# Kernel tuning notes

Hardware: AMD Instinct MI355X
Metric: run time of the kernel (lower is better)

## Reference

```python
import jax, jax.numpy as jnp
import numpy as np

B, S, E, H = 2, 2048, 1024, 16
D = E // H  # head_dim = 64


def _rope_angles(seq_len, d, dtype=jnp.float32):
    # standard RoPE frequencies: theta_i = 10000^{-2i/d}
    inv_freq = 1.0 / (10000.0 ** (jnp.arange(0, d, 2, dtype=dtype) / d))  # [d/2]
    pos = jnp.arange(seq_len, dtype=dtype)                                # [S]
    ang = pos[:, None] * inv_freq[None, :]                                # [S, d/2]
    ang = jnp.concatenate([ang, ang], axis=-1)                            # [S, d]
    return jnp.cos(ang), jnp.sin(ang)


def _rotate_half(t):
    t1, t2 = jnp.split(t, 2, axis=-1)
    return jnp.concatenate([-t2, t1], axis=-1)


def _apply_rope(t, cos, sin):
    # t: [B, H, S, D]; cos/sin: [S, D]
    return t * cos[None, None, :, :] + _rotate_half(t) * sin[None, None, :, :]


def setup_inputs() -> dict:
    key = jax.random.key(0)
    ks = jax.random.split(key, 6)
    x = jax.random.normal(ks[0], (B, S, E), dtype=jnp.float32)
    mask = jnp.tril(jnp.ones((S, S), dtype=bool))  # causal: True = attend
    scale = 1.0 / np.sqrt(E)
    Wq = jax.random.normal(ks[1], (E, E), dtype=jnp.float32) * scale
    Wk = jax.random.normal(ks[2], (E, E), dtype=jnp.float32) * scale
    Wv = jax.random.normal(ks[3], (E, E), dtype=jnp.float32) * scale
    Wo = jax.random.normal(ks[4], (E, E), dtype=jnp.float32) * scale
    z = jnp.zeros((E,), dtype=jnp.float32)
    return {"x": x, "mask": mask, "Wq": Wq, "bq": z, "Wk": Wk, "bk": z,
            "Wv": Wv, "bv": z, "Wo": Wo, "bo": z}


def reference(x, mask, Wq, bq, Wk, bk, Wv, bv, Wo, bo):
    b, s, e = x.shape
    # QKV projections (nn.Linear convention: y = x @ W.T + b)
    def proj(W, bias):
        y = jnp.einsum('bse,fe->bsf', x, W) + bias
        return y.reshape(b, s, H, D).transpose(0, 2, 1, 3)  # [B,H,S,D]
    q, k, v = proj(Wq, bq), proj(Wk, bk), proj(Wv, bv)
    # RoPE on q and k (per-head rotary over head_dim)
    cos, sin = _rope_angles(s, D, dtype=x.dtype)
    q = _apply_rope(q, cos, sin)
    k = _apply_rope(k, cos, sin)
    # SDPA with boolean mask (True = attend)
    scores = jnp.einsum('bhqd,bhkd->bhqk', q, k) / jnp.sqrt(jnp.asarray(D, x.dtype))
    neg = jnp.asarray(jnp.finfo(x.dtype).min, x.dtype)
    scores = jnp.where(mask[None, None, :, :], scores, neg)
    attn = jax.nn.softmax(scores, axis=-1)
    out = jnp.einsum('bhqk,bhkd->bhqd', attn, v)          # [B,H,S,D]
    out = out.transpose(0, 2, 1, 3).reshape(b, s, e)       # [B,S,E]
    return jnp.einsum('bse,fe->bsf', out, Wo) + bo
```

## Files before the change

### kernel.cpp

```cpp
#include <hip/hip_runtime.h>
#include <hip/hip_bf16.h>

typedef unsigned short u16;
typedef unsigned int u32;
typedef __bf16 bf16x8 __attribute__((ext_vector_type(8)));
typedef float f32x4 __attribute__((ext_vector_type(4)));

#define S_LEN 2048
#define NHEAD 16
#define HDIM  64
#define EMB   1024
#define BATCH 2

__device__ __forceinline__ float bf2f(u16 u) {
  union { unsigned int i; float f; } c; c.i = ((unsigned int)u) << 16; return c.f;
}
__device__ __forceinline__ u16 f2bf(float f) {
  union { float f; unsigned int i; } c; c.f = f;
  unsigned int i = c.i;
  return (u16)((i + 0x7FFFu + ((i >> 16) & 1u)) >> 16);
}
__device__ __forceinline__ u16 f2bf_trunc(float f) {
  union { float f; unsigned int i; } c; c.f = f;
  return (u16)(c.i >> 16);
}
__device__ __forceinline__ f32x4 mfma16(bf16x8 a, bf16x8 b, f32x4 c) {
  return __builtin_amdgcn_mfma_f32_16x16x32_bf16(a, b, c, 0, 0, 0);
}
__device__ __forceinline__ void cp16(const u16* g, u16* l) {
  __builtin_amdgcn_global_load_lds(
      (const __attribute__((address_space(1))) u32*)g,
      (__attribute__((address_space(3))) u32*)l, 16, 0, 0);
}

__global__ __launch_bounds__(256) void convert_kernel(
    const void* __restrict__ x, const void* __restrict__ Wq,
    const void* __restrict__ Wk, const void* __restrict__ Wv,
    const void* __restrict__ Wo,
    u16* __restrict__ xb, u16* __restrict__ wqb, u16* __restrict__ wkb,
    u16* __restrict__ wvb, u16* __restrict__ wob,
    int* __restrict__ flag, float2* __restrict__ tab)
{
  __shared__ int s_flag;
  if (threadIdx.x == 0) s_flag = 0;
  __syncthreads();
  {
    const u16* xs = (const u16*)x;
    u16 w0 = xs[threadIdx.x * 2], w1 = xs[threadIdx.x * 2 + 1];
    if ((((w0 >> 7) & 0xFF) >= 0xC0) || (((w1 >> 7) & 0xFF) >= 0xC0))
      atomicOr(&s_flag, 1);
  }
  __syncthreads();
  const int f32io = s_flag;
  if (blockIdx.x == 0 && threadIdx.x == 0) flag[0] = f32io;

  size_t gid = (size_t)blockIdx.x * 256 + threadIdx.x;
  size_t e = gid * 8;
  const void* src; u16* dst; size_t off;
  if (e < 4194304) { src = x; dst = xb; off = e; }
  else {
    size_t rr = e - 4194304;
    int j = (int)(rr >> 20); off = rr & 1048575;
    src = (j == 0) ? Wq : (j == 1) ? Wk : (j == 2) ? Wv : Wo;
    dst = (j == 0) ? wqb : (j == 1) ? wkb : (j == 2) ? wvb : wob;
  }
  if (f32io) {
    const float* s = (const float*)src + off;
    float4 a = *(const float4*)s;
    float4 b2 = *(const float4*)(s + 4);
    ushort4 u0; u0.x = f2bf(a.x); u0.y = f2bf(a.y); u0.z = f2bf(a.z); u0.w = f2bf(a.w);
    ushort4 u1; u1.x = f2bf(b2.x); u1.y = f2bf(b2.y); u1.z = f2bf(b2.z); u1.w = f2bf(b2.w);
    *(ushort4*)(dst + off) = u0;
    *(ushort4*)(dst + off + 4) = u1;
  } else {
    *(uint4*)(dst + off) = *(const uint4*)((const u16*)src + off);
  }

  if (blockIdx.x < 256) {
    int id = blockIdx.x * 256 + threadIdx.x;
    int s = id >> 5, i = id & 31;
    float f = exp2f(-(float)i * 0.41524101186092029f);
    float ang = (float)s * f;
    tab[id] = make_float2(cosf(ang), sinf(ang));
  }
}

__device__ __forceinline__ void gemm_core(
    const u16* __restrict__ A, const u16* __restrict__ W,
    int m0, int n0, int t, f32x4 (&acc)[4][4],
    u16 (&Ash)[128][32], u16 (&Bsh)[128][32])
{
  const int lane = t & 63, lr = lane & 15, quad = lane >> 4;
  const int wv = t >> 6;
  const int wm = (wv & 1) * 64, wn = (wv >> 1) * 64;
  for (int kt = 0; kt < 1024; kt += 32) {
    __syncthreads();
#pragma unroll
    for (int p = 0; p < 2; ++p) {
      const int i = t + p * 256;
      const int r = i >> 2, c = (i & 3) * 8;
      u16* la = &Ash[0][0] + (size_t)(p * 256 + (t & 192)) * 8;
      u16* lb = &Bsh[0][0] + (size_t)(p * 256 + (t & 192)) * 8;
      cp16(A + (size_t)(m0 + r) * 1024 + kt + c, la);
      cp16(W + (size_t)(n0 + r) * 1024 + kt + c, lb);
    }
    __syncthreads();
    bf16x8 af[4], bfr[4];
#pragma unroll
    for (int mi = 0; mi < 4; ++mi)
      af[mi] = *(const bf16x8*)&Ash[wm + mi * 16 + lr][quad * 8];
#pragma unroll
    for (int ni = 0; ni < 4; ++ni)
      bfr[ni] = *(const bf16x8*)&Bsh[wn + ni * 16 + lr][quad * 8];
#pragma unroll
    for (int mi = 0; mi < 4; ++mi)
#pragma unroll
      for (int ni = 0; ni < 4; ++ni)
        acc[mi][ni] = mfma16(af[mi], bfr[ni], acc[mi][ni]);
  }
}

__device__ __forceinline__ void gemm_epilogue(
    int mode, int f32io, f32x4 (&acc)[4][4],
    const void* biasvp, void* outvp, int m0, int n0, int t,
    const float2* __restrict__ tab)
{
  const int lane = t & 63, lr = lane & 15, quad = lane >> 4;
  const int wv = t >> 6;
  const int wm = (wv & 1) * 64, wn = (wv >> 1) * 64;
  const float* biasf = (const float*)biasvp;
  const u16* biasb = (const u16*)biasvp;
#define BIASV(n) (f32io ? biasf[(n)] : bf2f(biasb[(n)]))
  if (mode == 1) {
    u16* Out = (u16*)outvp;
#pragma unroll
    for (int mi = 0; mi < 4; ++mi) {
#pragma unroll
      for (int r = 0; r < 4; ++r) {
        int mm = m0 + wm + mi * 16 + quad * 4 + r;
        int s = mm & (S_LEN - 1), b = mm >> 11;
        float2 cs0 = tab[s * 32 + lr];
        float2 cs1 = tab[s * 32 + 16 + lr];
#pragma unroll
        for (int ni = 0; ni < 4; ++ni) {
          int n = n0 + wn + ni * 16 + lr;
          int h = n >> 6, d = n & 63;
          float v  = acc[mi][ni][r]     + BIASV(n);
          float vp = acc[mi][ni ^ 2][r] + BIASV(n ^ 32);
          float rot = (d < 32) ? -vp : vp;
          float cc = (ni & 1) ? cs1.x : cs0.x;
          float ss = (ni & 1) ? cs1.y : cs0.y;
          size_t off = (((size_t)(b * NHEAD + h)) * S_LEN + s) * HDIM + d;
          Out[off] = f2bf(v * cc + rot * ss);
        }
      }
    }
  } else if (mode == 2) {
    u16* Out = (u16*)outvp;
#pragma unroll
    for (int mi = 0; mi < 4; ++mi) {
      int mm = m0 + wm + mi * 16 + quad * 4;
      int s = mm & (S_LEN - 1), b = mm >> 11;
#pragma unroll
      for (int ni = 0; ni < 4; ++ni) {
        int n = n0 + wn + ni * 16 + lr;
        int h = n >> 6, d = n & 63;
        float bv = BIASV(n);
        u16 p0 = f2bf(acc[mi][ni][0] + bv);
        u16 p1 = f2bf(acc[mi][ni][1] + bv);
        u16 p2 = f2bf(acc[mi][ni][2] + bv);
        u16 p3 = f2bf(acc[mi][ni][3] + bv);
        uint2 pk = make_uint2((u32)p0 | ((u32)p1 << 16),
                              (u32)p2 | ((u32)p3 << 16));
        size_t off = (((size_t)(b * NHEAD + h)) * HDIM + d) * S_LEN + s;
        *(uint2*)(Out + off) = pk;
      }
    }
  }
#undef BIASV
}

__global__ __launch_bounds__(256) void gemm_qkv(
    const u16* __restrict__ A, const u16* __restrict__ Wq,
    const u16* __restrict__ Wk, const u16* __restrict__ Wv,
    const void* bq, const void* bk, const void* bv,
    u16* qo, u16* ko, u16* vo, const int* __restrict__ dflag,
    const float2* __restrict__ tab)
{
  alignas(16) __shared__ u16 Ash[128][32];
  alignas(16) __shared__ u16 Bsh[128][32];
  const int wsel = blockIdx.x >> 3;
  const u16* W = (wsel == 0) ? Wq : (wsel == 1) ? Wk : Wv;
  const void* bias = (wsel == 0) ? bq : (wsel == 1) ? bk : bv;
  void* out = (wsel == 0) ? (void*)qo : (wsel == 1) ? (void*)ko : (void*)vo;
  const int mode = (wsel == 2) ? 2 : 1;
  const int m0 = blockIdx.y * 128, n0 = (blockIdx.x & 7) * 128;
  f32x4 acc[4][4];
  const f32x4 zero4 = {0.f, 0.f, 0.f, 0.f};
#pragma unroll
  for (int i = 0; i < 4; ++i)
#pragma unroll
    for (int j = 0; j < 4; ++j) acc[i][j] = zero4;
  gemm_core(A, W, m0, n0, threadIdx.x, acc, Ash, Bsh);
  gemm_epilogue(mode, dflag[0], acc, bias, out, m0, n0, threadIdx.x, tab);
}

__global__ __launch_bounds__(256) void gemm_out(
    const u16* __restrict__ A, const u16* __restrict__ W,
    const void* bias, void* out, const int* __restrict__ dflag)
{
  alignas(16) __shared__ u16 SH[(64 + 128) * 32];
  const int t = threadIdx.x, lane = t & 63, wv = t >> 6;
  const int lr = lane & 15, quad = lane >> 4;
  const int m0 = blockIdx.y * 64, n0 = blockIdx.x * 128;
  const int wm = (wv & 1) * 32, wn = (wv >> 1) * 64;
  const int f32io = dflag[0];
  u16 (*Ash)[32] = (u16(*)[32])SH;
  u16 (*Bsh)[32] = (u16(*)[32])(SH + 64 * 32);

  f32x4 acc[2][4];
  const f32x4 zero4 = {0.f, 0.f, 0.f, 0.f};
#pragma unroll
  for (int i = 0; i < 2; ++i)
#pragma unroll
    for (int j = 0; j < 4; ++j) acc[i][j] = zero4;

  for (int kt = 0; kt < 1024; kt += 32) {
    __syncthreads();
#pragma unroll
    for (int p = 0; p < 3; ++p) {
      const int i = t + p * 256;
      u16* l = SH + (size_t)(p * 256 + (t & 192)) * 8;
      const u16* g;
      if (p == 0) {
        g = A + (size_t)(m0 + (i >> 2)) * 1024 + kt + (i & 3) * 8;
      } else {
        const int ib = i - 256;
        g = W + (size_t)(n0 + (ib >> 2)) * 1024 + kt + (ib & 3) * 8;
      }
      cp16(g, l);
    }
    __syncthreads();
    bf16x8 af[2], bfr[4];
#pragma unroll
    for (int mi = 0; mi < 2; ++mi)
      af[mi] = *(const bf16x8*)&Ash[wm + mi * 16 + lr][quad * 8];
#pragma unroll
    for (int ni = 0; ni < 4; ++ni)
      bfr[ni] = *(const bf16x8*)&Bsh[wn + ni * 16 + lr][quad * 8];
#pragma unroll
    for (int mi = 0; mi < 2; ++mi)
#pragma unroll
      for (int ni = 0; ni < 4; ++ni)
        acc[mi][ni] = mfma16(af[mi], bfr[ni], acc[mi][ni]);
  }

  const float* biasf = (const float*)bias;
  const u16* biasb = (const u16*)bias;
  float* Outf = (float*)out;
  u16* Outb = (u16*)out;
#pragma unroll
  for (int mi = 0; mi < 2; ++mi) {
#pragma unroll
    for (int r = 0; r < 4; ++r) {
      int mm = m0 + wm + mi * 16 + quad * 4 + r;
#pragma unroll
      for (int ni = 0; ni < 4; ++ni) {
        int n = n0 + wn + ni * 16 + lr;
        float bv = f32io ? biasf[n] : bf2f(biasb[n]);
        float v = acc[mi][ni][r] + bv;
        size_t off = (size_t)mm * 1024 + n;
        if (f32io) Outf[off] = v; else Outb[off] = f2bf(v);
      }
    }
  }
}

__device__ __forceinline__ void attn_phase(
    const bf16x8 (&qf)[2], f32x4 (&oacc)[4], float (&lsum)[4],
    u16 (&Ksh)[64][72], u16 (&Vsh)[64][72], u16 (&Psh)[4][16][72],
    int kv0, int q0w, bool diag, int lr, int quad, int wv)
{
  const f32x4 zero4 = {0.f, 0.f, 0.f, 0.f};
  f32x4 sc[4];
#pragma unroll
  for (int ni = 0; ni < 4; ++ni) {
    bf16x8 kf0 = *(const bf16x8*)&Ksh[ni * 16 + lr][quad * 8];
    bf16x8 kf1 = *(const bf16x8*)&Ksh[ni * 16 + lr][32 + quad * 8];
    f32x4 z = zero4;
    z = mfma16(qf[0], kf0, z);
    z = mfma16(qf[1], kf1, z);
    sc[ni] = z;
  }
  if (diag) {
#pragma unroll
    for (int ni = 0; ni < 4; ++ni)
#pragma unroll
      for (int r = 0; r < 4; ++r) {
        float sarg = sc[ni][r] * 0.18033688f - 21.64042561f;
        if (kv0 + ni * 16 + lr > q0w + quad * 4 + r) sarg = -1e4f;
        float p = exp2f(sarg);
        sc[ni][r] = p;
        lsum[r] += p;
      }
  } else {
#pragma unroll
    for (int ni = 0; ni < 4; ++ni)
#pragma unroll
      for (int r = 0; r < 4; ++r) {
        float p = exp2f(sc[ni][r] * 0.18033688f - 21.64042561f);
        sc[ni][r] = p;
        lsum[r] += p;
      }
  }
#pragma unroll
  for (int ni = 0; ni < 4; ++ni)
#pragma unroll
    for (int r = 0; r < 4; ++r)
      Psh[wv][quad * 4 + r][ni * 16 + lr] = f2bf_trunc(sc[ni][r]);
  bf16x8 pa0 = *(const bf16x8*)&Psh[wv][lr][quad * 8];
  bf16x8 pa1 = *(const bf16x8*)&Psh[wv][lr][32 + quad * 8];
#pragma unroll
  for (int oni = 0; oni < 4; ++oni) {
    bf16x8 vf0 = *(const bf16x8*)&Vsh[oni * 16 + lr][quad * 8];
    bf16x8 vf1 = *(const bf16x8*)&Vsh[oni * 16 + lr][32 + quad * 8];
    oacc[oni] = mfma16(pa0, vf0, oacc[oni]);
    oacc[oni] = mfma16(pa1, vf1, oacc[oni]);
  }
}

__device__ __forceinline__ void attn_finish(
    f32x4 (&oacc)[4], float (&lsum)[4], u16* __restrict__ O,
    int bh, int q0w, int lr, int quad)
{
  const int b = bh >> 4, h = bh & 15;
#pragma unroll
  for (int r = 0; r < 4; ++r) {
#pragma unroll
    for (int off = 1; off < 16; off <<= 1) lsum[r] += __shfl_xor(lsum[r], off);
    lsum[r] = 1.f / lsum[r];
  }
#pragma unroll
  for (int oni = 0; oni < 4; ++oni)
#pragma unroll
    for (int r = 0; r < 4; ++r) {
      int s = q0w + quad * 4 + r;
      int e = h * HDIM + oni * 16 + lr;
      O[((size_t)(b * S_LEN + s)) * EMB + e] = f2bf(oacc[oni][r] * lsum[r]);
    }
}

__global__ __launch_bounds__(256) void attn_kernel(
    const u16* __restrict__ Q, const u16* __restrict__ Kr,
    const u16* __restrict__ Vt, u16* __restrict__ O)
{
  alignas(16) __shared__ u16 Ksh[64][72];
  alignas(16) __shared__ u16 Vsh[64][72];
  alignas(16) __shared__ u16 Psh[4][16][72];
  const int t = threadIdx.x, lane = t & 63, wv = t >> 6;
  const int lr = lane & 15, quad = lane >> 4;
  const int bh = blockIdx.y;
  const int qtA = blockIdx.x;
  const int qtB = 31 - qtA;
  const int qA0 = qtA * 64 + wv * 16;
  const int qB0 = qtB * 64 + wv * 16;
  const size_t base = (size_t)bh * S_LEN * HDIM;

  bf16x8 qfA[2], qfB[2];
  {
    const u16* ra = Q + base + (size_t)(qA0 + lr) * HDIM + quad * 8;
    qfA[0] = *(const bf16x8*)ra; qfA[1] = *(const bf16x8*)(ra + 32);
    const u16* rb = Q + base + (size_t)(qB0 + lr) * HDIM + quad * 8;
    qfB[0] = *(const bf16x8*)rb; qfB[1] = *(const bf16x8*)(rb + 32);
  }

  f32x4 oaccA[4], oaccB[4];
  float lsA[4], lsB[4];
  const f32x4 zero4 = {0.f, 0.f, 0.f, 0.f};
#pragma unroll
  for (int i = 0; i < 4; ++i) {
    oaccA[i] = zero4; oaccB[i] = zero4; lsA[i] = 0.f; lsB[i] = 0.f;
  }

  const int jmax = qtB;
  for (int j = 0; j <= jmax; ++j) {
    const int kv0 = j * 64;
    __syncthreads();
#pragma unroll
    for (int p = 0; p < 2; ++p) {
      int c = t + p * 256;
      int r = c >> 3, cc = (c & 7) * 8;
      *(uint4*)&Ksh[r][cc] = *(const uint4*)(Kr + base + (size_t)(kv0 + r) * HDIM + cc);
      *(uint4*)&Vsh[r][cc] = *(const uint4*)(Vt + base + (size_t)r * S_LEN + kv0 + cc);
    }
    __syncthreads();
    if (j <= qtA)
      attn_phase(qfA, oaccA, lsA, Ksh, Vsh, Psh, kv0, qA0, j == qtA, lr, quad, wv);
    attn_phase(qfB, oaccB, lsB, Ksh, Vsh, Psh, kv0, qB0, j == jmax, lr, quad, wv);
  }

  attn_finish(oaccA, lsA, O, bh, qA0, lr, quad);
  attn_finish(oaccB, lsB, O, bh, qB0, lr, quad);
}

extern "C" void kernel_launch(void* const* d_in, const int* in_sizes, int n_in,
                              void* d_out, int out_size, void* d_ws, size_t ws_size,
                              hipStream_t stream) {
  const void* x  = d_in[0];
  const void* Wq = d_in[2]; const void* bq = d_in[3];
  const void* Wk = d_in[4]; const void* bk = d_in[5];
  const void* Wv = d_in[6]; const void* bv = d_in[7];
  const void* Wo = d_in[8]; const void* bo = d_in[9];

  char* ws = (char*)d_ws;
  int* flag = (int*)ws;
  u16* xb  = (u16*)(ws + 256);
  u16* qws = xb  + 4194304;
  u16* kws = qws + 4194304;
  u16* vws = kws + 4194304;
  u16* wqb = vws + 4194304;
  u16* wkb = wqb + 1048576;
  u16* wvb = wkb + 1048576;
  u16* wob = wvb + 1048576;
  float2* tab = (float2*)(wob + 1048576);
  u16* ows = xb;

  convert_kernel<<<4096, 256, 0, stream>>>(x, Wq, Wk, Wv, Wo,
                                           xb, wqb, wkb, wvb, wob, flag, tab);
  gemm_qkv<<<dim3(24, 32), 256, 0, stream>>>(xb, wqb, wkb, wvb,
                                             bq, bk, bv, qws, kws, vws, flag, tab);
  attn_kernel<<<dim3(16, 32), 256, 0, stream>>>(qws, kws, vws, ows);
  gemm_out<<<dim3(8, 64), 256, 0, stream>>>(ows, wob, bo, d_out, flag);
}
```

Baseline: 245.6 us.

## Register-prefetch GEMM tiles and split attention query tiles across 512-thread blocks

Both GEMM kernels stop using direct global-to-LDS copies. They now prefetch the next K-slice into registers while the current slice is consumed, then store it to LDS at the top of the next iteration, so global latency overlaps with MFMA work. The attention kernel goes from 256 to 512 threads: the first four waves handle the short query tile and the last four the long one, instead of each wave processing both tiles in sequence. This adds register pressure and extra LDS store instructions in the GEMMs. In attention, the waves on the short tile sit idle for the remaining iterations but still take part in every barrier.

Measured after the change: 240.3 us. -2.1%, faster.

```diff
diff --git a/kernel.cpp b/kernel.cpp
--- a/kernel.cpp
+++ b/kernel.cpp
@@ -26,11 +26,6 @@
 }
 __device__ __forceinline__ f32x4 mfma16(bf16x8 a, bf16x8 b, f32x4 c) {
   return __builtin_amdgcn_mfma_f32_16x16x32_bf16(a, b, c, 0, 0, 0);
-}
-__device__ __forceinline__ void cp16(const u16* g, u16* l) {
-  __builtin_amdgcn_global_load_lds(
-      (const __attribute__((address_space(1))) u32*)g,
-      (__attribute__((address_space(3))) u32*)l, 16, 0, 0);
 }
 
 __global__ __launch_bounds__(256) void convert_kernel(
@@ -85,33 +80,43 @@
   }
 }
 
-__device__ __forceinline__ void gemm_core(
+__device__ __forceinline__ void gemm_core_pipe(
     const u16* __restrict__ A, const u16* __restrict__ W,
     int m0, int n0, int t, f32x4 (&acc)[4][4],
-    u16 (&Ash)[128][32], u16 (&Bsh)[128][32])
+    u16* __restrict__ Ash, u16* __restrict__ Bsh)
 {
   const int lane = t & 63, lr = lane & 15, quad = lane >> 4;
   const int wv = t >> 6;
   const int wm = (wv & 1) * 64, wn = (wv >> 1) * 64;
+  const int i0 = t, i1 = t + 256;
+  const u16* gA0 = A + (size_t)(m0 + (i0 >> 2)) * 1024 + (i0 & 3) * 8;
+  const u16* gA1 = A + (size_t)(m0 + (i1 >> 2)) * 1024 + (i1 & 3) * 8;
+  const u16* gB0 = W + (size_t)(n0 + (i0 >> 2)) * 1024 + (i0 & 3) * 8;
+  const u16* gB1 = W + (size_t)(n0 + (i1 >> 2)) * 1024 + (i1 & 3) * 8;
+  uint4 ra0 = *(const uint4*)gA0;
+  uint4 ra1 = *(const uint4*)gA1;
+  uint4 rb0 = *(const uint4*)gB0;
+  uint4 rb1 = *(const uint4*)gB1;
   for (int kt = 0; kt < 1024; kt += 32) {
     __syncthreads();
-#pragma unroll
-    for (int p = 0; p < 2; ++p) {
-      const int i = t + p * 256;
-      const int r = i >> 2, c = (i & 3) * 8;
-      u16* la = &Ash[0][0] + (size_t)(p * 256 + (t & 192)) * 8;
-      u16* lb = &Bsh[0][0] + (size_t)(p * 256 + (t & 192)) * 8;
-      cp16(A + (size_t)(m0 + r) * 1024 + kt + c, la);
-      cp16(W + (size_t)(n0 + r) * 1024 + kt + c, lb);
-    }
-    __syncthreads();
+    *(uint4*)(Ash + (size_t)i0 * 8) = ra0;
+    *(uint4*)(Ash + (size_t)i1 * 8) = ra1;
+    *(uint4*)(Bsh + (size_t)i0 * 8) = rb0;
+    *(uint4*)(Bsh + (size_t)i1 * 8) = rb1;
+    __syncthreads();
+    if (kt + 32 < 1024) {
+      ra0 = *(const uint4*)(gA0 + kt + 32);
+      ra1 = *(const uint4*)(gA1 + kt + 32);
+      rb0 = *(const uint4*)(gB0 + kt + 32);
+      rb1 = *(const uint4*)(gB1 + kt + 32);
+    }
     bf16x8 af[4], bfr[4];
 #pragma unroll
     for (int mi = 0; mi < 4; ++mi)
-      af[mi] = *(const bf16x8*)&Ash[wm + mi * 16 + lr][quad * 8];
+      af[mi] = *(const bf16x8*)(Ash + (size_t)(wm + mi * 16 + lr) * 32 + quad * 8);
 #pragma unroll
     for (int ni = 0; ni < 4; ++ni)
-      bfr[ni] = *(const bf16x8*)&Bsh[wn + ni * 16 + lr][quad * 8];
+      bfr[ni] = *(const bf16x8*)(Bsh + (size_t)(wn + ni * 16 + lr) * 32 + quad * 8);
 #pragma unroll
     for (int mi = 0; mi < 4; ++mi)
 #pragma unroll
@@ -187,8 +192,8 @@
     u16* qo, u16* ko, u16* vo, const int* __restrict__ dflag,
     const float2* __restrict__ tab)
 {
-  alignas(16) __shared__ u16 Ash[128][32];
-  alignas(16) __shared__ u16 Bsh[128][32];
+  alignas(16) __shared__ u16 Ash[128 * 32];
+  alignas(16) __shared__ u16 Bsh[128 * 32];
   const int wsel = blockIdx.x >> 3;
   const u16* W = (wsel == 0) ? Wq : (wsel == 1) ? Wk : Wv;
   const void* bias = (wsel == 0) ? bq : (wsel == 1) ? bk : bv;
@@ -201,7 +206,7 @@
   for (int i = 0; i < 4; ++i)
 #pragma unroll
     for (int j = 0; j < 4; ++j) acc[i][j] = zero4;
-  gemm_core(A, W, m0, n0, threadIdx.x, acc, Ash, Bsh);
+  gemm_core_pipe(A, W, m0, n0, threadIdx.x, acc, Ash, Bsh);
   gemm_epilogue(mode, dflag[0], acc, bias, out, m0, n0, threadIdx.x, tab);
 }
 
@@ -209,14 +214,20 @@
     const u16* __restrict__ A, const u16* __restrict__ W,
     const void* bias, void* out, const int* __restrict__ dflag)
 {
-  alignas(16) __shared__ u16 SH[(64 + 128) * 32];
+  alignas(16) __shared__ u16 Ash[64 * 32];
+  alignas(16) __shared__ u16 Bsh[128 * 32];
   const int t = threadIdx.x, lane = t & 63, wv = t >> 6;
   const int lr = lane & 15, quad = lane >> 4;
   const int m0 = blockIdx.y * 64, n0 = blockIdx.x * 128;
   const int wm = (wv & 1) * 32, wn = (wv >> 1) * 64;
   const int f32io = dflag[0];
-  u16 (*Ash)[32] = (u16(*)[32])SH;
-  u16 (*Bsh)[32] = (u16(*)[32])(SH + 64 * 32);
+  const int i0 = t, i1 = t + 256;
+  const u16* gA0 = A + (size_t)(m0 + (i0 >> 2)) * 1024 + (i0 & 3) * 8;
+  const u16* gB0 = W + (size_t)(n0 + (i0 >> 2)) * 1024 + (i0 & 3) * 8;
+  const u16* gB1 = W + (size_t)(n0 + (i1 >> 2)) * 1024 + (i1 & 3) * 8;
+  uint4 ra0 = *(const uint4*)gA0;
+  uint4 rb0 = *(const uint4*)gB0;
+  uint4 rb1 = *(const uint4*)gB1;
 
   f32x4 acc[2][4];
   const f32x4 zero4 = {0.f, 0.f, 0.f, 0.f};
@@ -227,27 +238,22 @@
 
   for (int kt = 0; kt < 1024; kt += 32) {
     __syncthreads();
-#pragma unroll
-    for (int p = 0; p < 3; ++p) {
-      const int i = t + p * 256;
-      u16* l = SH + (size_t)(p * 256 + (t & 192)) * 8;
-      const u16* g;
-      if (p == 0) {
-        g = A + (size_t)(m0 + (i >> 2)) * 1024 + kt + (i & 3) * 8;
-      } else {
-        const int ib = i - 256;
-        g = W + (size_t)(n0 + (ib >> 2)) * 1024 + kt + (ib & 3) * 8;
-      }
-      cp16(g, l);
-    }
-    __syncthreads();
+    *(uint4*)(Ash + (size_t)i0 * 8) = ra0;
+    *(uint4*)(Bsh + (size_t)i0 * 8) = rb0;
+    *(uint4*)(Bsh + (size_t)i1 * 8) = rb1;
+    __syncthreads();
+    if (kt + 32 < 1024) {
+      ra0 = *(const uint4*)(gA0 + kt + 32);
+      rb0 = *(const uint4*)(gB0 + kt + 32);
+      rb1 = *(const uint4*)(gB1 + kt + 32);
+    }
     bf16x8 af[2], bfr[4];
 #pragma unroll
     for (int mi = 0; mi < 2; ++mi)
-      af[mi] = *(const bf16x8*)&Ash[wm + mi * 16 + lr][quad * 8];
+      af[mi] = *(const bf16x8*)(Ash + (size_t)(wm + mi * 16 + lr) * 32 + quad * 8);
 #pragma unroll
     for (int ni = 0; ni < 4; ++ni)
-      bfr[ni] = *(const bf16x8*)&Bsh[wn + ni * 16 + lr][quad * 8];
+      bfr[ni] = *(const bf16x8*)(Bsh + (size_t)(wn + ni * 16 + lr) * 32 + quad * 8);
 #pragma unroll
     for (int mi = 0; mi < 2; ++mi)
 #pragma unroll
@@ -278,7 +284,7 @@
 
 __device__ __forceinline__ void attn_phase(
     const bf16x8 (&qf)[2], f32x4 (&oacc)[4], float (&lsum)[4],
-    u16 (&Ksh)[64][72], u16 (&Vsh)[64][72], u16 (&Psh)[4][16][72],
+    u16 (&Ksh)[64][72], u16 (&Vsh)[64][72], u16 (&Psh)[8][16][72],
     int kv0, int q0w, bool diag, int lr, int quad, int wv)
 {
   const f32x4 zero4 = {0.f, 0.f, 0.f, 0.f};
@@ -350,57 +356,50 @@
     }
 }
 
-__global__ __launch_bounds__(256) void attn_kernel(
+__global__ __launch_bounds__(512) void attn_kernel(
     const u16* __restrict__ Q, const u16* __restrict__ Kr,
     const u16* __restrict__ Vt, u16* __restrict__ O)
 {
   alignas(16) __shared__ u16 Ksh[64][72];
   alignas(16) __shared__ u16 Vsh[64][72];
-  alignas(16) __shared__ u16 Psh[4][16][72];
+  alignas(16) __shared__ u16 Psh[8][16][72];
   const int t = threadIdx.x, lane = t & 63, wv = t >> 6;
   const int lr = lane & 15, quad = lane >> 4;
   const int bh = blockIdx.y;
   const int qtA = blockIdx.x;
   const int qtB = 31 - qtA;
-  const int qA0 = qtA * 64 + wv * 16;
-  const int qB0 = qtB * 64 + wv * 16;
+  const int myTile = (wv < 4) ? qtA : qtB;
+  const int q0w = myTile * 64 + (wv & 3) * 16;
   const size_t base = (size_t)bh * S_LEN * HDIM;
 
-  bf16x8 qfA[2], qfB[2];
+  bf16x8 qf[2];
   {
-    const u16* ra = Q + base + (size_t)(qA0 + lr) * HDIM + quad * 8;
-    qfA[0] = *(const bf16x8*)ra; qfA[1] = *(const bf16x8*)(ra + 32);
-    const u16* rb = Q + base + (size_t)(qB0 + lr) * HDIM + quad * 8;
-    qfB[0] = *(const bf16x8*)rb; qfB[1] = *(const bf16x8*)(rb + 32);
-  }
-
-  f32x4 oaccA[4], oaccB[4];
-  float lsA[4], lsB[4];
+    const u16* qrow = Q + base + (size_t)(q0w + lr) * HDIM + quad * 8;
+    qf[0] = *(const bf16x8*)qrow;
+    qf[1] = *(const bf16x8*)(qrow + 32);
+  }
+
+  f32x4 oacc[4];
+  float lsum[4];
   const f32x4 zero4 = {0.f, 0.f, 0.f, 0.f};
 #pragma unroll
-  for (int i = 0; i < 4; ++i) {
-    oaccA[i] = zero4; oaccB[i] = zero4; lsA[i] = 0.f; lsB[i] = 0.f;
-  }
+  for (int i = 0; i < 4; ++i) { oacc[i] = zero4; lsum[i] = 0.f; }
 
   const int jmax = qtB;
   for (int j = 0; j <= jmax; ++j) {
     const int kv0 = j * 64;
     __syncthreads();
-#pragma unroll
-    for (int p = 0; p < 2; ++p) {
-      int c = t + p * 256;
-      int r = c >> 3, cc = (c & 7) * 8;
+    {
+      int r = t >> 3, cc = (t & 7) * 8;
       *(uint4*)&Ksh[r][cc] = *(const uint4*)(Kr + base + (size_t)(kv0 + r) * HDIM + cc);
       *(uint4*)&Vsh[r][cc] = *(const uint4*)(Vt + base + (size_t)r * S_LEN + kv0 + cc);
     }
     __syncthreads();
-    if (j <= qtA)
-      attn_phase(qfA, oaccA, lsA, Ksh, Vsh, Psh, kv0, qA0, j == qtA, lr, quad, wv);
-    attn_phase(qfB, oaccB, lsB, Ksh, Vsh, Psh, kv0, qB0, j == jmax, lr, quad, wv);
-  }
-
-  attn_finish(oaccA, lsA, O, bh, qA0, lr, quad);
-  attn_finish(oaccB, lsB, O, bh, qB0, lr, quad);
+    if (j <= myTile)
+      attn_phase(qf, oacc, lsum, Ksh, Vsh, Psh, kv0, q0w, j == myTile, lr, quad, wv);
+  }
+
+  attn_finish(oacc, lsum, O, bh, q0w, lr, quad);
 }
 
 extern "C" void kernel_launch(void* const* d_in, const int* in_sizes, int n_in,
@@ -429,6 +428,6 @@
                                            xb, wqb, wkb, wvb, wob, flag, tab);
   gemm_qkv<<<dim3(24, 32), 256, 0, stream>>>(xb, wqb, wkb, wvb,
                                              bq, bk, bv, qws, kws, vws, flag, tab);
-  attn_kernel<<<dim3(16, 32), 256, 0, stream>>>(qws, kws, vws, ows);
+  attn_kernel<<<dim3(16, 32), 512, 0, stream>>>(qws, kws, vws, ows);
   gemm_out<<<dim3(8, 64), 256, 0, stream>>>(ows, wob, bo, d_out, flag);
 }
```
